# Performance work log

Measured on AMD Instinct MI355X. Metric: run time of the kernel, lower is better.

Reference implementation:

```python
import jax, jax.numpy as jnp
import numpy as np

B, N, K = 64, 1024, 16  # graphs per batch, nodes per graph, top-k (k=16 hardcoded in module)
EPS = 1e-20


def setup_inputs() -> dict:
    key = jax.random.key(0)
    ks = jax.random.split(key, 6)
    C = 128
    x = jax.random.normal(ks[0], (B * N, C), jnp.float32)
    pos = jax.random.normal(ks[1], (B * N, 3), jnp.float32)
    W1 = jax.random.normal(ks[2], (C, C), jnp.float32) / np.sqrt(C).astype(np.float32)
    b1 = jnp.zeros((C,), jnp.float32)
    gamma = jnp.ones((C,), jnp.float32)
    beta = jnp.zeros((C,), jnp.float32)
    W2 = jax.random.normal(ks[3], (C, 10), jnp.float32) / np.sqrt(C).astype(np.float32)
    b2 = jnp.zeros((10,), jnp.float32)
    t = jnp.ones((1,), jnp.float32)
    return dict(x=x, pos=pos, W1=W1, b1=b1, gamma=gamma, beta=beta, W2=W2, b2=b2, t=t)


def _edge_arrays(idx):
    # idx: (B, N, K) per-target top-k source node indices (graph-local)
    offs = (jnp.arange(B, dtype=jnp.int32) * N)[:, None, None]
    src = (idx + offs).reshape(-1)
    tgt = (jnp.broadcast_to(jnp.arange(N, dtype=jnp.int32)[None, :, None], (B, N, K)) + offs).reshape(-1)
    return jnp.stack([src, tgt])  # (2, B*N*K)


def _knn_edges(pos):
    # KNNGraph(k=16) on positions, loop=False (exclude self)
    p = pos.reshape(B, N, 3)
    d2 = jnp.sum((p[:, :, None, :] - p[:, None, :, :]) ** 2, axis=-1)  # (B,N,N)
    d2 = d2 + jnp.eye(N, dtype=d2.dtype) * 1e10
    _, idx = jax.lax.top_k(-d2, K)  # nearest K per node
    return _edge_arrays(idx)


def reference(x, pos, W1, b1, gamma, beta, W2, b2, t):
    key = jax.random.key(42)
    k1, k2 = jax.random.split(key)
    # tg MLP: lin -> batchnorm -> relu -> lin (training-mode batch stats over nodes)
    h = x @ W1 + b1
    mu = h.mean(axis=0)
    var = h.var(axis=0)
    h = (h - mu) / jnp.sqrt(var + 1e-5) * gamma + beta
    h = jax.nn.relu(h)
    emb = h @ W2 + b2  # (B*N, 10)
    emb = emb + jax.random.uniform(k1, emb.shape, emb.dtype) * 0.001
    e = emb.reshape(B, N, 10)
    # pairwise distances per graph (vectorized over the python loop in the original)
    diff = e[:, :, None, :] - e[:, None, :, :]  # (B,N,N,10)
    dist = jnp.linalg.norm(diff, axis=-1)  # (B,N,N)
    p = jnp.exp(-t[0] * dist ** 2)
    u = jax.random.uniform(k2, p.shape, p.dtype)
    gumbel = -jnp.log(-jnp.log(u + EPS) + EPS)
    noisy_logits = jnp.log(p + EPS) + gumbel
    # torch topk over dim=0 (sources) for each target column -> transpose then top_k on last axis
    vals, idx = jax.lax.top_k(jnp.swapaxes(noisy_logits, 1, 2), K)  # (B,N,K)
    vals = jax.nn.softmax(vals, axis=-1)
    vals = vals / vals.max(axis=-1, keepdims=True)
    soft_idx = _edge_arrays(idx)  # (2, B*N*K)
    knn_idx = _knn_edges(pos)
    edge_index = jnp.concatenate([soft_idx, knn_idx], axis=1)
    return vals.reshape(-1), soft_idx, edge_index
```

## Files before the change

### kernel.cpp

```cpp
#include <hip/hip_runtime.h>
#include <stdint.h>
#include <math.h>

#define BG 64
#define NG 1024
#define KK 16
#define CC 128
#define NNODE (BG * NG)
#define NSOFT (BG * NG * KK)
#define FEPS 1e-20f

__host__ __device__ __forceinline__ uint32_t rotl32u(uint32_t x, int r) {
  return (x << r) | (x >> (32 - r));
}

__host__ __device__ __forceinline__ void tf2x32(uint32_t k0, uint32_t k1,
                                                uint32_t x0, uint32_t x1,
                                                uint32_t &o0, uint32_t &o1) {
  uint32_t k2 = k0 ^ k1 ^ 0x1BD11BDAu;
  x0 += k0; x1 += k1;
#define TFR(r) { x0 += x1; x1 = rotl32u(x1, r); x1 ^= x0; }
  TFR(13) TFR(15) TFR(26) TFR(6)
  x0 += k1; x1 += k2 + 1u;
  TFR(17) TFR(29) TFR(16) TFR(24)
  x0 += k2; x1 += k0 + 2u;
  TFR(13) TFR(15) TFR(26) TFR(6)
  x0 += k0; x1 += k1 + 3u;
  TFR(17) TFR(29) TFR(16) TFR(24)
  x0 += k1; x1 += k2 + 4u;
  TFR(13) TFR(15) TFR(26) TFR(6)
  x0 += k2; x1 += k0 + 5u;
#undef TFR
  o0 = x0; o1 = x1;
}

__device__ __forceinline__ float jax_uniform01(uint32_t ka, uint32_t kb, uint32_t m) {
  uint32_t o0, o1;
  tf2x32(ka, kb, 0u, m, o0, o1);
  uint32_t bits = o0 ^ o1;
  float f = __uint_as_float((bits >> 9) | 0x3f800000u) - 1.0f;
  return fmaxf(f, 0.0f);
}

__device__ __forceinline__ int vbin_soft(float v) {
  float fb = (v + 50.0f) * (256.0f / 67.0f);
  fb = fminf(fmaxf(fb, 0.0f), 255.0f);
  return (int)fb;
}
__device__ __forceinline__ int vbin_knn(float v) {
  float fb = (v + 64.0f) * 4.0f;
  fb = fminf(fmaxf(fb, 0.0f), 255.0f);
  return (int)fb;
}

#define LDS_WAIT() asm volatile("s_waitcnt lgkmcnt(0)" ::: "memory")

__global__ __launch_bounds__(256) void k_gemm1(const float* __restrict__ x,
                                               const float* __restrict__ W1,
                                               const float* __restrict__ b1,
                                               float* __restrict__ h,
                                               float* __restrict__ p1,
                                               float* __restrict__ p2) {
  __shared__ __align__(16) float xs[64 * 128];
  const int t = threadIdx.x;
  const size_t blockBase = (size_t)blockIdx.x * (64 * 128);
  #pragma unroll
  for (int j = 0; j < 32; ++j) xs[t + j * 256] = x[blockBase + t + j * 256];
  __syncthreads();
  const int c = t & 127;
  const int rg = t >> 7;
  float acc[32];
  #pragma unroll
  for (int j = 0; j < 32; ++j) acc[j] = 0.f;
  const float* xrow = &xs[rg * 32 * 128];
  for (int k4 = 0; k4 < 128; k4 += 4) {
    const float w0 = W1[(size_t)(k4 + 0) * 128 + c];
    const float w1 = W1[(size_t)(k4 + 1) * 128 + c];
    const float w2 = W1[(size_t)(k4 + 2) * 128 + c];
    const float w3 = W1[(size_t)(k4 + 3) * 128 + c];
    #pragma unroll
    for (int j = 0; j < 32; ++j) {
      const float4 xv = *(const float4*)&xrow[j * 128 + k4];
      acc[j] = fmaf(xv.x, w0, acc[j]);
      acc[j] = fmaf(xv.y, w1, acc[j]);
      acc[j] = fmaf(xv.z, w2, acc[j]);
      acc[j] = fmaf(xv.w, w3, acc[j]);
    }
  }
  const float bb = b1[c];
  float s1 = 0.f, s2 = 0.f;
  #pragma unroll
  for (int j = 0; j < 32; ++j) {
    const float v = acc[j] + bb;
    h[blockBase + (size_t)(rg * 32 + j) * 128 + c] = v;
    s1 += v;
    s2 = fmaf(v, v, s2);
  }
  __syncthreads();
  float* r1 = xs;
  float* r2 = xs + 256;
  r1[rg * 128 + c] = s1;
  r2[rg * 128 + c] = s2;
  __syncthreads();
  if (t < 128) {
    p1[(size_t)t * 1024 + blockIdx.x] = r1[t] + r1[128 + t];
  } else {
    const int cc = t - 128;
    p2[(size_t)cc * 1024 + blockIdx.x] = r2[cc] + r2[128 + cc];
  }
}

__global__ __launch_bounds__(256) void k_bn_final(const float* __restrict__ p1,
                                                  const float* __restrict__ p2,
                                                  const float* __restrict__ gamma,
                                                  const float* __restrict__ beta,
                                                  float* __restrict__ scale,
                                                  float* __restrict__ shift) {
  const int c = blockIdx.x, t = threadIdx.x;
  const float* q1 = p1 + (size_t)c * 1024;
  const float* q2 = p2 + (size_t)c * 1024;
  float a1 = q1[t] + q1[t + 256] + q1[t + 512] + q1[t + 768];
  float a2 = q2[t] + q2[t + 256] + q2[t + 512] + q2[t + 768];
  __shared__ float r1[256], r2[256];
  r1[t] = a1; r2[t] = a2;
  __syncthreads();
  for (int o = 128; o > 0; o >>= 1) {
    if (t < o) { r1[t] += r1[t + o]; r2[t] += r2[t + o]; }
    __syncthreads();
  }
  if (t == 0) {
    const float mu = r1[0] * (1.0f / NNODE);
    float var = r2[0] * (1.0f / NNODE) - mu * mu;
    var = fmaxf(var, 0.f);
    const float sc = gamma[c] / sqrtf(var + 1e-5f);
    scale[c] = sc;
    shift[c] = beta[c] - mu * sc;
  }
}

__global__ __launch_bounds__(256) void k_emb(const float* __restrict__ h,
                                             const float* __restrict__ scale,
                                             const float* __restrict__ shift,
                                             const float* __restrict__ W2,
                                             const float* __restrict__ b2,
                                             float* __restrict__ e,
                                             uint32_t ka, uint32_t kb) {
  __shared__ __align__(16) float hn[64 * 132];
  const int t = threadIdx.x;
  const int rowBase = blockIdx.x * 64;
  {
    const int c = t & 127;
    const float sc = scale[c], sh = shift[c];
    #pragma unroll
    for (int j = 0; j < 32; ++j) {
      const int r = (t >> 7) + j * 2;
      const float v = fmaf(h[(size_t)(rowBase + r) * 128 + c], sc, sh);
      hn[r * 132 + c] = fmaxf(v, 0.f);
    }
  }
  __syncthreads();
  #pragma unroll
  for (int j = 0; j < 3; ++j) {
    const int o = t + j * 256;
    if (o < 640) {
      const int r = o / 10;
      const int col = o - r * 10;
      float acc = 0.f;
      for (int k4 = 0; k4 < 128; k4 += 4) {
        const float4 hv = *(const float4*)&hn[r * 132 + k4];
        acc = fmaf(hv.x, W2[(k4 + 0) * 10 + col], acc);
        acc = fmaf(hv.y, W2[(k4 + 1) * 10 + col], acc);
        acc = fmaf(hv.z, W2[(k4 + 2) * 10 + col], acc);
        acc = fmaf(hv.w, W2[(k4 + 3) * 10 + col], acc);
      }
      acc += b2[col];
      const uint32_t m = (uint32_t)(rowBase + r) * 10u + (uint32_t)col;
      const float u = jax_uniform01(ka, kb, m);
      e[(size_t)(rowBase + r) * 10 + col] = acc + u * 0.001f;
    }
  }
}

__global__ __launch_bounds__(512) void k_soft(const float* __restrict__ e,
                                              const float* __restrict__ tsc,
                                              float* __restrict__ out,
                                              uint32_t ka, uint32_t kb) {
  __shared__ float    els[10 * NG];
  __shared__ uint32_t bins[8][256];
  __shared__ float    cv[8][48];
  __shared__ int      cidx[8][48];
  __shared__ uint32_t cnt[8];
  __shared__ float    o16v[8][16];
  __shared__ int      o16i[8][16];

  const int t = threadIdx.x, lane = t & 63, w = t >> 6;
  const int node = blockIdx.x * 8 + w;
  const int b = blockIdx.x >> 7;
  const int jt = node & (NG - 1);
  const float negt = -tsc[0];
  const float* eg = e + (size_t)b * (NG * 10);

  { uint4 z = {0, 0, 0, 0}; *(uint4*)&bins[w][lane * 4] = z; }
  if (lane == 0) cnt[w] = 0u;

  for (int s = t; s < NG; s += 512) {
    const float2* rp = (const float2*)(eg + (size_t)s * 10);
    const float2 a0 = rp[0], a1 = rp[1], a2 = rp[2], a3 = rp[3], a4 = rp[4];
    els[0 * NG + s] = a0.x; els[1 * NG + s] = a0.y;
    els[2 * NG + s] = a1.x; els[3 * NG + s] = a1.y;
    els[4 * NG + s] = a2.x; els[5 * NG + s] = a2.y;
    els[6 * NG + s] = a3.x; els[7 * NG + s] = a3.y;
    els[8 * NG + s] = a4.x; els[9 * NG + s] = a4.y;
  }
  __syncthreads();

  float ej[10];
  #pragma unroll
  for (int d = 0; d < 10; ++d) ej[d] = els[d * NG + jt];

  float vv[16];
  const uint32_t mL = ((uint32_t)b << 20) + (uint32_t)jt + ((uint32_t)lane << 10);
  #pragma unroll
  for (int st = 0; st < 16; ++st) {
    const int s = st * 64 + lane;
    float dd, acc;
    dd = ej[0] - els[0 * NG + s]; acc = dd * dd;
    dd = ej[1] - els[1 * NG + s]; acc = fmaf(dd, dd, acc);
    dd = ej[2] - els[2 * NG + s]; acc = fmaf(dd, dd, acc);
    dd = ej[3] - els[3 * NG + s]; acc = fmaf(dd, dd, acc);
    dd = ej[4] - els[4 * NG + s]; acc = fmaf(dd, dd, acc);
    dd = ej[5] - els[5 * NG + s]; acc = fmaf(dd, dd, acc);
    dd = ej[6] - els[6 * NG + s]; acc = fmaf(dd, dd, acc);
    dd = ej[7] - els[7 * NG + s]; acc = fmaf(dd, dd, acc);
    dd = ej[8] - els[8 * NG + s]; acc = fmaf(dd, dd, acc);
    dd = ej[9] - els[9 * NG + s]; acc = fmaf(dd, dd, acc);
    const float dist = sqrtf(acc);
    const float d2 = dist * dist;
    const float p = __expf(negt * d2);
    const float u = jax_uniform01(ka, kb, mL + ((uint32_t)st << 16));
    const float li = __logf(u + FEPS);
    const float g = -__logf(FEPS - li);
    const float v = __logf(p + FEPS) + g;
    vv[st] = v;
    atomicAdd(&bins[w][vbin_soft(v)], 1u);
  }
  LDS_WAIT();

  const uint4 c4 = *(const uint4*)&bins[w][lane * 4];
  const uint32_t lsum = c4.x + c4.y + c4.z + c4.w;
  uint32_t xs = lsum;
  #pragma unroll
  for (int off = 1; off < 64; off <<= 1) {
    uint32_t tt = (uint32_t)__shfl_down((int)xs, off, 64);
    if (lane + off < 64) xs += tt;
  }
  const uint32_t after = xs - lsum;
  const uint32_t s3 = c4.w + after;
  const uint32_t s2 = c4.z + s3;
  const uint32_t s1 = c4.y + s2;
  const uint32_t s0 = c4.x + s1;
  int localB = -1;
  if (s3 >= 16u) localB = lane * 4 + 3;
  else if (s2 >= 16u) localB = lane * 4 + 2;
  else if (s1 >= 16u) localB = lane * 4 + 1;
  else if (s0 >= 16u) localB = lane * 4 + 0;
  const unsigned long long msk = __ballot(localB >= 0);
  const int hl = 63 - __builtin_clzll(msk);
  const int B = __shfl(localB, hl, 64);

  #pragma unroll
  for (int st = 0; st < 16; ++st) {
    if (vbin_soft(vv[st]) >= B) {
      const uint32_t pos = atomicAdd(&cnt[w], 1u);
      if (pos < 48u) { cv[w][pos] = vv[st]; cidx[w][pos] = st * 64 + lane; }
    }
  }
  LDS_WAIT();

  int C = (int)cnt[w]; if (C > 48) C = 48;
  const float mvv = (lane < C) ? cv[w][lane] : 0.f;
  const int   mii = (lane < C) ? cidx[w][lane] : 0;
  int rank = 0;
  for (int j = 0; j < C; ++j) {
    const float vj = cv[w][j];
    const int ij = cidx[w][j];
    if (vj > mvv || (vj == mvv && ij < mii)) ++rank;
  }
  if (lane < C && rank < 16) { o16v[w][rank] = mvv; o16i[w][rank] = mii; }
  LDS_WAIT();

  if (lane < 16) {
    const float vq = o16v[w][lane];
    const float m0 = o16v[w][0];
    float uex = __expf(vq - m0);
    float ss = uex;
    #pragma unroll
    for (int off = 1; off < 16; off <<= 1) ss += __shfl_xor(ss, off, 16);
    const float u0 = __shfl(uex, 0, 16);
    const float s0v = u0 / ss;
    const float sv = uex / ss;
    const float o = sv / s0v;
    const size_t base = (size_t)node * KK + lane;
    const float tgtf = (float)node;
    const float srcf = (float)(b * NG + o16i[w][lane]);
    out[base] = o;
    out[(size_t)NSOFT + base] = srcf;
    out[2 * (size_t)NSOFT + base] = tgtf;
    out[3 * (size_t)NSOFT + base] = srcf;
    out[5 * (size_t)NSOFT + base] = tgtf;
  }
}

__global__ __launch_bounds__(512) void k_knn(const float* __restrict__ pos,
                                             float* __restrict__ out) {
  __shared__ float    pls[3 * NG];
  __shared__ uint32_t bins[8][256];
  __shared__ float    cv[8][48];
  __shared__ int      cidx[8][48];
  __shared__ uint32_t cnt[8];
  __shared__ int      o16i[8][16];

  const int t = threadIdx.x, lane = t & 63, w = t >> 6;
  const int node = blockIdx.x * 8 + w;
  const int b = blockIdx.x >> 7;
  const int it = node & (NG - 1);
  const float* pg = pos + (size_t)b * (NG * 3);

  { uint4 z = {0, 0, 0, 0}; *(uint4*)&bins[w][lane * 4] = z; }
  if (lane == 0) cnt[w] = 0u;

  for (int s = t; s < NG; s += 512) {
    pls[0 * NG + s] = pg[(size_t)s * 3 + 0];
    pls[1 * NG + s] = pg[(size_t)s * 3 + 1];
    pls[2 * NG + s] = pg[(size_t)s * 3 + 2];
  }
  __syncthreads();

  const float px = pls[0 * NG + it];
  const float py = pls[1 * NG + it];
  const float pz = pls[2 * NG + it];

  float vv[16];
  #pragma unroll
  for (int st = 0; st < 16; ++st) {
    const int s = st * 64 + lane;
    const float dx = px - pls[0 * NG + s];
    const float dy = py - pls[1 * NG + s];
    const float dz = pz - pls[2 * NG + s];
    float d2 = dx * dx;
    d2 = fmaf(dy, dy, d2);
    d2 = fmaf(dz, dz, d2);
    if (s == it) d2 += 1e10f;
    const float v = -d2;
    vv[st] = v;
    atomicAdd(&bins[w][vbin_knn(v)], 1u);
  }
  LDS_WAIT();

  const uint4 c4 = *(const uint4*)&bins[w][lane * 4];
  const uint32_t lsum = c4.x + c4.y + c4.z + c4.w;
  uint32_t xs = lsum;
  #pragma unroll
  for (int off = 1; off < 64; off <<= 1) {
    uint32_t tt = (uint32_t)__shfl_down((int)xs, off, 64);
    if (lane + off < 64) xs += tt;
  }
  const uint32_t after = xs - lsum;
  const uint32_t s3 = c4.w + after;
  const uint32_t s2 = c4.z + s3;
  const uint32_t s1 = c4.y + s2;
  const uint32_t s0 = c4.x + s1;
  int localB = -1;
  if (s3 >= 16u) localB = lane * 4 + 3;
  else if (s2 >= 16u) localB = lane * 4 + 2;
  else if (s1 >= 16u) localB = lane * 4 + 1;
  else if (s0 >= 16u) localB = lane * 4 + 0;
  const unsigned long long msk = __ballot(localB >= 0);
  const int hl = 63 - __builtin_clzll(msk);
  const int B = __shfl(localB, hl, 64);

  #pragma unroll
  for (int st = 0; st < 16; ++st) {
    if (vbin_knn(vv[st]) >= B) {
      const uint32_t pos = atomicAdd(&cnt[w], 1u);
      if (pos < 48u) { cv[w][pos] = vv[st]; cidx[w][pos] = st * 64 + lane; }
    }
  }
  LDS_WAIT();

  int C = (int)cnt[w]; if (C > 48) C = 48;
  const float mvv = (lane < C) ? cv[w][lane] : 0.f;
  const int   mii = (lane < C) ? cidx[w][lane] : 0;
  int rank = 0;
  for (int j = 0; j < C; ++j) {
    const float vj = cv[w][j];
    const int ij = cidx[w][j];
    if (vj > mvv || (vj == mvv && ij < mii)) ++rank;
  }
  if (lane < C && rank < 16) o16i[w][rank] = mii;
  LDS_WAIT();

  if (lane < 16) {
    const size_t base = (size_t)node * KK + lane;
    out[4 * (size_t)NSOFT + base] = (float)(b * NG + o16i[w][lane]);
    out[6 * (size_t)NSOFT + base] = (float)node;
  }
}

extern "C" void kernel_launch(void* const* d_in, const int* in_sizes, int n_in,
                              void* d_out, int out_size, void* d_ws, size_t ws_size,
                              hipStream_t stream) {
  const float* x     = (const float*)d_in[0];
  const float* pos   = (const float*)d_in[1];
  const float* W1    = (const float*)d_in[2];
  const float* b1    = (const float*)d_in[3];
  const float* gamma = (const float*)d_in[4];
  const float* beta  = (const float*)d_in[5];
  const float* W2    = (const float*)d_in[6];
  const float* b2    = (const float*)d_in[7];
  const float* t     = (const float*)d_in[8];
  float* out = (float*)d_out;

  float* ws    = (float*)d_ws;
  float* h     = ws;
  float* e     = h + (size_t)NNODE * CC;
  float* p1    = e + (size_t)NNODE * 10;
  float* p2    = p1 + 128 * 1024;
  float* scale = p2 + 128 * 1024;
  float* shift = scale + CC;

  uint32_t k1a, k1b, k2a, k2b;
  tf2x32(0u, 42u, 0u, 0u, k1a, k1b);
  tf2x32(0u, 42u, 0u, 1u, k2a, k2b);

  k_gemm1<<<dim3(NNODE / 64), dim3(256), 0, stream>>>(x, W1, b1, h, p1, p2);
  k_bn_final<<<dim3(CC), dim3(256), 0, stream>>>(p1, p2, gamma, beta, scale, shift);
  k_emb<<<dim3(NNODE / 64), dim3(256), 0, stream>>>(h, scale, shift, W2, b2, e, k1a, k1b);
  k_knn<<<dim3(NNODE / 8), dim3(512), 0, stream>>>(pos, out);
  k_soft<<<dim3(NNODE / 8), dim3(512), 0, stream>>>(e, t, out, k2a, k2b);
}
```

Baseline: 419.8 us.

## Process two target nodes per wavefront in soft top-k kernel

The soft kernel now has each wavefront handle two target columns, so every source embedding read from shared memory is reused for two distance computations. Embeddings are stored as float2 pairs for wider LDS loads, and the grid is halved. The per-column histogram and select logic is duplicated through a macro. This adds register pressure (two sets of 16 values plus two query vectors), which may lower occupancy, while the Gumbel RNG and transcendental work per element stays the same.

Result: slower. 440.9 us (+5.0%).

```diff
diff --git a/kernel.cpp b/kernel.cpp
--- a/kernel.cpp
+++ b/kernel.cpp
@@ -185,64 +185,217 @@
                                               const float* __restrict__ tsc,
                                               float* __restrict__ out,
                                               uint32_t ka, uint32_t kb) {
-  __shared__ float    els[10 * NG];
+  __shared__ __align__(16) float2 els2[5 * NG];
+  __shared__ uint32_t bins[8][2][256];
+  __shared__ float    cv[8][2][48];
+  __shared__ int      cidx[8][2][48];
+  __shared__ uint32_t cnt[8][2];
+  __shared__ float    o16v[8][2][16];
+  __shared__ int      o16i[8][2][16];
+
+  const int t = threadIdx.x, lane = t & 63, w = t >> 6;
+  const int b = blockIdx.x >> 6;
+  const int tbase = (blockIdx.x & 63) << 4;
+  const int jt0 = tbase + w * 2, jt1 = jt0 + 1;
+  const float negt = -tsc[0];
+  const float* eg = e + (size_t)b * (NG * 10);
+
+  { uint4 z = {0, 0, 0, 0};
+    *(uint4*)&bins[w][0][lane * 4] = z;
+    *(uint4*)&bins[w][1][lane * 4] = z; }
+  if (lane == 0) { cnt[w][0] = 0u; cnt[w][1] = 0u; }
+
+  for (int s = t; s < NG; s += 512) {
+    const float2* rp = (const float2*)(eg + (size_t)s * 10);
+    els2[0 * NG + s] = rp[0];
+    els2[1 * NG + s] = rp[1];
+    els2[2 * NG + s] = rp[2];
+    els2[3 * NG + s] = rp[3];
+    els2[4 * NG + s] = rp[4];
+  }
+  __syncthreads();
+
+  float ej0[10], ej1[10];
+  #pragma unroll
+  for (int p = 0; p < 5; ++p) {
+    const float2 a = els2[p * NG + jt0];
+    const float2 c = els2[p * NG + jt1];
+    ej0[2 * p] = a.x; ej0[2 * p + 1] = a.y;
+    ej1[2 * p] = c.x; ej1[2 * p + 1] = c.y;
+  }
+
+  float vv0[16], vv1[16];
+  const uint32_t mA = ((uint32_t)b << 20) + ((uint32_t)lane << 10) + (uint32_t)jt0;
+  const uint32_t mBt = mA + 1u;
+  #pragma unroll 4
+  for (int st = 0; st < 16; ++st) {
+    const int s = st * 64 + lane;
+    const float2 r0 = els2[0 * NG + s];
+    const float2 r1 = els2[1 * NG + s];
+    const float2 r2 = els2[2 * NG + s];
+    const float2 r3 = els2[3 * NG + s];
+    const float2 r4 = els2[4 * NG + s];
+    float dd, a0, a1;
+    dd = ej0[0] - r0.x; a0 = dd * dd;
+    dd = ej0[1] - r0.y; a0 = fmaf(dd, dd, a0);
+    dd = ej0[2] - r1.x; a0 = fmaf(dd, dd, a0);
+    dd = ej0[3] - r1.y; a0 = fmaf(dd, dd, a0);
+    dd = ej0[4] - r2.x; a0 = fmaf(dd, dd, a0);
+    dd = ej0[5] - r2.y; a0 = fmaf(dd, dd, a0);
+    dd = ej0[6] - r3.x; a0 = fmaf(dd, dd, a0);
+    dd = ej0[7] - r3.y; a0 = fmaf(dd, dd, a0);
+    dd = ej0[8] - r4.x; a0 = fmaf(dd, dd, a0);
+    dd = ej0[9] - r4.y; a0 = fmaf(dd, dd, a0);
+    dd = ej1[0] - r0.x; a1 = dd * dd;
+    dd = ej1[1] - r0.y; a1 = fmaf(dd, dd, a1);
+    dd = ej1[2] - r1.x; a1 = fmaf(dd, dd, a1);
+    dd = ej1[3] - r1.y; a1 = fmaf(dd, dd, a1);
+    dd = ej1[4] - r2.x; a1 = fmaf(dd, dd, a1);
+    dd = ej1[5] - r2.y; a1 = fmaf(dd, dd, a1);
+    dd = ej1[6] - r3.x; a1 = fmaf(dd, dd, a1);
+    dd = ej1[7] - r3.y; a1 = fmaf(dd, dd, a1);
+    dd = ej1[8] - r4.x; a1 = fmaf(dd, dd, a1);
+    dd = ej1[9] - r4.y; a1 = fmaf(dd, dd, a1);
+    {
+      const float dist = sqrtf(a0);
+      const float d2 = dist * dist;
+      const float p = __expf(negt * d2);
+      const float u = jax_uniform01(ka, kb, mA + ((uint32_t)st << 16));
+      const float li = __logf(u + FEPS);
+      const float g = -__logf(FEPS - li);
+      const float v = __logf(p + FEPS) + g;
+      vv0[st] = v;
+      atomicAdd(&bins[w][0][vbin_soft(v)], 1u);
+    }
+    {
+      const float dist = sqrtf(a1);
+      const float d2 = dist * dist;
+      const float p = __expf(negt * d2);
+      const float u = jax_uniform01(ka, kb, mBt + ((uint32_t)st << 16));
+      const float li = __logf(u + FEPS);
+      const float g = -__logf(FEPS - li);
+      const float v = __logf(p + FEPS) + g;
+      vv1[st] = v;
+      atomicAdd(&bins[w][1][vbin_soft(v)], 1u);
+    }
+  }
+  LDS_WAIT();
+
+#define FINALIZE(TT, JT, VV)                                                   \
+  {                                                                            \
+    const uint4 c4 = *(const uint4*)&bins[w][TT][lane * 4];                    \
+    const uint32_t lsum = c4.x + c4.y + c4.z + c4.w;                           \
+    uint32_t xs = lsum;                                                        \
+    _Pragma("unroll")                                                          \
+    for (int off = 1; off < 64; off <<= 1) {                                   \
+      uint32_t tt2 = (uint32_t)__shfl_down((int)xs, off, 64);                  \
+      if (lane + off < 64) xs += tt2;                                          \
+    }                                                                          \
+    const uint32_t after = xs - lsum;                                          \
+    const uint32_t s3 = c4.w + after;                                          \
+    const uint32_t s2 = c4.z + s3;                                             \
+    const uint32_t s1 = c4.y + s2;                                             \
+    const uint32_t s0 = c4.x + s1;                                             \
+    int localB = -1;                                                           \
+    if (s3 >= 16u) localB = lane * 4 + 3;                                      \
+    else if (s2 >= 16u) localB = lane * 4 + 2;                                 \
+    else if (s1 >= 16u) localB = lane * 4 + 1;                                 \
+    else if (s0 >= 16u) localB = lane * 4 + 0;                                 \
+    const unsigned long long msk = __ballot(localB >= 0);                      \
+    const int hl = 63 - __builtin_clzll(msk);                                  \
+    const int B = __shfl(localB, hl, 64);                                      \
+    _Pragma("unroll")                                                          \
+    for (int st = 0; st < 16; ++st) {                                          \
+      if (vbin_soft(VV[st]) >= B) {                                            \
+        const uint32_t pos = atomicAdd(&cnt[w][TT], 1u);                       \
+        if (pos < 48u) { cv[w][TT][pos] = VV[st];                              \
+                         cidx[w][TT][pos] = st * 64 + lane; }                  \
+      }                                                                        \
+    }                                                                          \
+    LDS_WAIT();                                                                \
+    int C = (int)cnt[w][TT]; if (C > 48) C = 48;                               \
+    const float mvv = (lane < C) ? cv[w][TT][lane] : 0.f;                      \
+    const int   mii = (lane < C) ? cidx[w][TT][lane] : 0;                      \
+    int rank = 0;                                                              \
+    for (int j = 0; j < C; ++j) {                                              \
+      const float vj = cv[w][TT][j];                                           \
+      const int ij = cidx[w][TT][j];                                           \
+      if (vj > mvv || (vj == mvv && ij < mii)) ++rank;                         \
+    }                                                                          \
+    if (lane < C && rank < 16) { o16v[w][TT][rank] = mvv;                      \
+                                 o16i[w][TT][rank] = mii; }                    \
+    LDS_WAIT();                                                                \
+    if (lane < 16) {                                                           \
+      const float vq = o16v[w][TT][lane];                                      \
+      const float m0 = o16v[w][TT][0];                                         \
+      float uex = __expf(vq - m0);                                             \
+      float ss = uex;                                                          \
+      _Pragma("unroll")                                                        \
+      for (int off = 1; off < 16; off <<= 1) ss += __shfl_xor(ss, off, 16);    \
+      const float u0 = __shfl(uex, 0, 16);                                     \
+      const float s0v = u0 / ss;                                               \
+      const float sv = uex / ss;                                               \
+      const float o = sv / s0v;                                                \
+      const int node = b * NG + (JT);                                          \
+      const size_t base = (size_t)node * KK + lane;                            \
+      const float tgtf = (float)node;                                          \
+      const float srcf = (float)(b * NG + o16i[w][TT][lane]);                  \
+      out[base] = o;                                                           \
+      out[(size_t)NSOFT + base] = srcf;                                        \
+      out[2 * (size_t)NSOFT + base] = tgtf;                                    \
+      out[3 * (size_t)NSOFT + base] = srcf;                                    \
+      out[5 * (size_t)NSOFT + base] = tgtf;                                    \
+    }                                                                          \
+  }
+
+  FINALIZE(0, jt0, vv0)
+  FINALIZE(1, jt1, vv1)
+#undef FINALIZE
+}
+
+__global__ __launch_bounds__(512) void k_knn(const float* __restrict__ pos,
+                                             float* __restrict__ out) {
+  __shared__ float    pls[3 * NG];
   __shared__ uint32_t bins[8][256];
   __shared__ float    cv[8][48];
   __shared__ int      cidx[8][48];
   __shared__ uint32_t cnt[8];
-  __shared__ float    o16v[8][16];
   __shared__ int      o16i[8][16];
 
   const int t = threadIdx.x, lane = t & 63, w = t >> 6;
   const int node = blockIdx.x * 8 + w;
   const int b = blockIdx.x >> 7;
-  const int jt = node & (NG - 1);
-  const float negt = -tsc[0];
-  const float* eg = e + (size_t)b * (NG * 10);
+  const int it = node & (NG - 1);
+  const float* pg = pos + (size_t)b * (NG * 3);
 
   { uint4 z = {0, 0, 0, 0}; *(uint4*)&bins[w][lane * 4] = z; }
   if (lane == 0) cnt[w] = 0u;
 
   for (int s = t; s < NG; s += 512) {
-    const float2* rp = (const float2*)(eg + (size_t)s * 10);
-    const float2 a0 = rp[0], a1 = rp[1], a2 = rp[2], a3 = rp[3], a4 = rp[4];
-    els[0 * NG + s] = a0.x; els[1 * NG + s] = a0.y;
-    els[2 * NG + s] = a1.x; els[3 * NG + s] = a1.y;
-    els[4 * NG + s] = a2.x; els[5 * NG + s] = a2.y;
-    els[6 * NG + s] = a3.x; els[7 * NG + s] = a3.y;
-    els[8 * NG + s] = a4.x; els[9 * NG + s] = a4.y;
-  }
-  __syncthreads();
-
-  float ej[10];
-  #pragma unroll
-  for (int d = 0; d < 10; ++d) ej[d] = els[d * NG + jt];
+    pls[0 * NG + s] = pg[(size_t)s * 3 + 0];
+    pls[1 * NG + s] = pg[(size_t)s * 3 + 1];
+    pls[2 * NG + s] = pg[(size_t)s * 3 + 2];
+  }
+  __syncthreads();
+
+  const float px = pls[0 * NG + it];
+  const float py = pls[1 * NG + it];
+  const float pz = pls[2 * NG + it];
 
   float vv[16];
-  const uint32_t mL = ((uint32_t)b << 20) + (uint32_t)jt + ((uint32_t)lane << 10);
   #pragma unroll
   for (int st = 0; st < 16; ++st) {
     const int s = st * 64 + lane;
-    float dd, acc;
-    dd = ej[0] - els[0 * NG + s]; acc = dd * dd;
-    dd = ej[1] - els[1 * NG + s]; acc = fmaf(dd, dd, acc);
-    dd = ej[2] - els[2 * NG + s]; acc = fmaf(dd, dd, acc);
-    dd = ej[3] - els[3 * NG + s]; acc = fmaf(dd, dd, acc);
-    dd = ej[4] - els[4 * NG + s]; acc = fmaf(dd, dd, acc);
-    dd = ej[5] - els[5 * NG + s]; acc = fmaf(dd, dd, acc);
-    dd = ej[6] - els[6 * NG + s]; acc = fmaf(dd, dd, acc);
-    dd = ej[7] - els[7 * NG + s]; acc = fmaf(dd, dd, acc);
-    dd = ej[8] - els[8 * NG + s]; acc = fmaf(dd, dd, acc);
-    dd = ej[9] - els[9 * NG + s]; acc = fmaf(dd, dd, acc);
-    const float dist = sqrtf(acc);
-    const float d2 = dist * dist;
-    const float p = __expf(negt * d2);
-    const float u = jax_uniform01(ka, kb, mL + ((uint32_t)st << 16));
-    const float li = __logf(u + FEPS);
-    const float g = -__logf(FEPS - li);
-    const float v = __logf(p + FEPS) + g;
+    const float dx = px - pls[0 * NG + s];
+    const float dy = py - pls[1 * NG + s];
+    const float dz = pz - pls[2 * NG + s];
+    float d2 = dx * dx;
+    d2 = fmaf(dy, dy, d2);
+    d2 = fmaf(dz, dz, d2);
+    if (s == it) d2 += 1e10f;
+    const float v = -d2;
     vv[st] = v;
-    atomicAdd(&bins[w][vbin_soft(v)], 1u);
+    atomicAdd(&bins[w][vbin_knn(v)], 1u);
   }
   LDS_WAIT();
 
@@ -270,117 +423,6 @@
 
   #pragma unroll
   for (int st = 0; st < 16; ++st) {
-    if (vbin_soft(vv[st]) >= B) {
-      const uint32_t pos = atomicAdd(&cnt[w], 1u);
-      if (pos < 48u) { cv[w][pos] = vv[st]; cidx[w][pos] = st * 64 + lane; }
-    }
-  }
-  LDS_WAIT();
-
-  int C = (int)cnt[w]; if (C > 48) C = 48;
-  const float mvv = (lane < C) ? cv[w][lane] : 0.f;
-  const int   mii = (lane < C) ? cidx[w][lane] : 0;
-  int rank = 0;
-  for (int j = 0; j < C; ++j) {
-    const float vj = cv[w][j];
-    const int ij = cidx[w][j];
-    if (vj > mvv || (vj == mvv && ij < mii)) ++rank;
-  }
-  if (lane < C && rank < 16) { o16v[w][rank] = mvv; o16i[w][rank] = mii; }
-  LDS_WAIT();
-
-  if (lane < 16) {
-    const float vq = o16v[w][lane];
-    const float m0 = o16v[w][0];
-    float uex = __expf(vq - m0);
-    float ss = uex;
-    #pragma unroll
-    for (int off = 1; off < 16; off <<= 1) ss += __shfl_xor(ss, off, 16);
-    const float u0 = __shfl(uex, 0, 16);
-    const float s0v = u0 / ss;
-    const float sv = uex / ss;
-    const float o = sv / s0v;
-    const size_t base = (size_t)node * KK + lane;
-    const float tgtf = (float)node;
-    const float srcf = (float)(b * NG + o16i[w][lane]);
-    out[base] = o;
-    out[(size_t)NSOFT + base] = srcf;
-    out[2 * (size_t)NSOFT + base] = tgtf;
-    out[3 * (size_t)NSOFT + base] = srcf;
-    out[5 * (size_t)NSOFT + base] = tgtf;
-  }
-}
-
-__global__ __launch_bounds__(512) void k_knn(const float* __restrict__ pos,
-                                             float* __restrict__ out) {
-  __shared__ float    pls[3 * NG];
-  __shared__ uint32_t bins[8][256];
-  __shared__ float    cv[8][48];
-  __shared__ int      cidx[8][48];
-  __shared__ uint32_t cnt[8];
-  __shared__ int      o16i[8][16];
-
-  const int t = threadIdx.x, lane = t & 63, w = t >> 6;
-  const int node = blockIdx.x * 8 + w;
-  const int b = blockIdx.x >> 7;
-  const int it = node & (NG - 1);
-  const float* pg = pos + (size_t)b * (NG * 3);
-
-  { uint4 z = {0, 0, 0, 0}; *(uint4*)&bins[w][lane * 4] = z; }
-  if (lane == 0) cnt[w] = 0u;
-
-  for (int s = t; s < NG; s += 512) {
-    pls[0 * NG + s] = pg[(size_t)s * 3 + 0];
-    pls[1 * NG + s] = pg[(size_t)s * 3 + 1];
-    pls[2 * NG + s] = pg[(size_t)s * 3 + 2];
-  }
-  __syncthreads();
-
-  const float px = pls[0 * NG + it];
-  const float py = pls[1 * NG + it];
-  const float pz = pls[2 * NG + it];
-
-  float vv[16];
-  #pragma unroll
-  for (int st = 0; st < 16; ++st) {
-    const int s = st * 64 + lane;
-    const float dx = px - pls[0 * NG + s];
-    const float dy = py - pls[1 * NG + s];
-    const float dz = pz - pls[2 * NG + s];
-    float d2 = dx * dx;
-    d2 = fmaf(dy, dy, d2);
-    d2 = fmaf(dz, dz, d2);
-    if (s == it) d2 += 1e10f;
-    const float v = -d2;
-    vv[st] = v;
-    atomicAdd(&bins[w][vbin_knn(v)], 1u);
-  }
-  LDS_WAIT();
-
-  const uint4 c4 = *(const uint4*)&bins[w][lane * 4];
-  const uint32_t lsum = c4.x + c4.y + c4.z + c4.w;
-  uint32_t xs = lsum;
-  #pragma unroll
-  for (int off = 1; off < 64; off <<= 1) {
-    uint32_t tt = (uint32_t)__shfl_down((int)xs, off, 64);
-    if (lane + off < 64) xs += tt;
-  }
-  const uint32_t after = xs - lsum;
-  const uint32_t s3 = c4.w + after;
-  const uint32_t s2 = c4.z + s3;
-  const uint32_t s1 = c4.y + s2;
-  const uint32_t s0 = c4.x + s1;
-  int localB = -1;
-  if (s3 >= 16u) localB = lane * 4 + 3;
-  else if (s2 >= 16u) localB = lane * 4 + 2;
-  else if (s1 >= 16u) localB = lane * 4 + 1;
-  else if (s0 >= 16u) localB = lane * 4 + 0;
-  const unsigned long long msk = __ballot(localB >= 0);
-  const int hl = 63 - __builtin_clzll(msk);
-  const int B = __shfl(localB, hl, 64);
-
-  #pragma unroll
-  for (int st = 0; st < 16; ++st) {
     if (vbin_knn(vv[st]) >= B) {
       const uint32_t pos = atomicAdd(&cnt[w], 1u);
       if (pos < 48u) { cv[w][pos] = vv[st]; cidx[w][pos] = st * 64 + lane; }
@@ -437,5 +479,5 @@
   k_bn_final<<<dim3(CC), dim3(256), 0, stream>>>(p1, p2, gamma, beta, scale, shift);
   k_emb<<<dim3(NNODE / 64), dim3(256), 0, stream>>>(h, scale, shift, W2, b2, e, k1a, k1b);
   k_knn<<<dim3(NNODE / 8), dim3(512), 0, stream>>>(pos, out);
-  k_soft<<<dim3(NNODE / 8), dim3(512), 0, stream>>>(e, t, out, k2a, k2b);
-}
+  k_soft<<<dim3(NNODE / 16), dim3(512), 0, stream>>>(e, t, out, k2a, k2b);
+}
```
